# Kernel optimization log

Measured on AMD Instinct MI355X. Metric: run time of the kernel, lower is better.

Reference implementation:

```python
import jax, jax.numpy as jnp
import numpy as np

EPS = 1e-4  # F.normalize eps


def setup_inputs() -> dict:
    key = jax.random.key(0)
    k1, k2, k3, k4 = jax.random.split(key, 4)
    return {
        "pred_feat": jax.random.normal(k1, (8192, 6), dtype=jnp.float32),
        "pred_decoder": jax.random.normal(k2, (4096, 4), dtype=jnp.float32),
        "input_data": jax.random.normal(k3, (4096, 4), dtype=jnp.float32),
        "gt_data": jax.random.normal(k4, (32768, 6), dtype=jnp.float32),
    }


def _normalize(x, eps=EPS):
    # torch F.normalize: x / max(||x||, eps)
    n = jnp.linalg.norm(x, axis=1, keepdims=True)
    return x / jnp.maximum(n, eps)


def reference(pred_feat, pred_decoder, input_data, gt_data):
    # train_decoder=False path (default inference/encoder-training path)
    pred_points = pred_feat[:, :3]    # [N,3]
    pred_normals = pred_feat[:, 3:]   # [N,3]
    gt_points = gt_data[:, :3]        # [L,3]
    gt_normals = gt_data[:, 3:]       # [L,3]

    # Squared Euclidean distances; argmin over squared == argmin over cdist(p=2).
    # dists2: [N, L] -- the big memory-bound intermediate
    p2 = jnp.sum(pred_points * pred_points, axis=1, keepdims=True)   # [N,1]
    g2 = jnp.sum(gt_points * gt_points, axis=1)                       # [L]
    dists2 = p2 - 2.0 * (pred_points @ gt_points.T) + g2[None, :]
    min_indices = jnp.argmin(dists2, axis=1)                          # [N]

    matched_pts = gt_points[min_indices]                              # [N,3]
    inlier_loss = jnp.mean((pred_points - matched_pts) ** 2)

    matched_nrm = gt_normals[min_indices]                             # [N,3]
    cos_theta = jnp.sum(_normalize(pred_normals) * _normalize(matched_nrm), axis=1)
    norm_loss = jnp.mean(1.0 - cos_theta)

    return inlier_loss + norm_loss
```

## Files before the change

kernel.cpp:

```cpp
#include <hip/hip_runtime.h>
#include <float.h>

#define NPRED 8192
#define NGT   32768
#define BLK   256
#define P     8
#define NCHUNK (NPRED / (BLK * P))
#define NSEG   128
#define SEGLEN (NGT / NSEG)
#define G      4
#define NGRP   (SEGLEN / G)
#define NPB    (NPRED / BLK)


__global__ void prep_kernel(const float* __restrict__ gt, float4* __restrict__ gt4,
                            unsigned long long* __restrict__ res) {
    int j = blockIdx.x * blockDim.x + threadIdx.x;
    if (j < NGT) {
        float x = gt[j * 6 + 0], y = gt[j * 6 + 1], z = gt[j * 6 + 2];
        gt4[j] = make_float4(-2.0f * x, -2.0f * y, -2.0f * z, x * x + y * y + z * z);
    }
    if (j < NPRED) res[j] = 0xFFFFFFFFFFFFFFFFull;
}

__device__ __forceinline__ unsigned int fkey(float f) {
    unsigned int u = __float_as_uint(f);
    return u ^ (unsigned int)(((int)u >> 31) | 0x80000000);
}

__device__ __forceinline__ float score(const float4& g, float px, float py, float pz) {
    return fmaf(g.x, px, fmaf(g.y, py, fmaf(g.z, pz, g.w)));
}

__global__ __launch_bounds__(BLK, 2) void argmin_kernel(const float* __restrict__ pred,
                                                        const float4* __restrict__ gt4,
                                                        unsigned long long* __restrict__ res) {
    __shared__ float4 tile[SEGLEN];
    const int t = threadIdx.x;
    const int chunk = blockIdx.x;
    const int seg = blockIdx.y;
    const int j0 = seg * SEGLEN;

    tile[t] = gt4[j0 + t];

    float px[P], py[P], pz[P], best[P];
    int bg[P];
    const int pbase = chunk * (BLK * P) + t;
    #pragma unroll
    for (int k = 0; k < P; ++k) {
        const float* p = pred + (size_t)(pbase + k * BLK) * 6;
        px[k] = p[0]; py[k] = p[1]; pz[k] = p[2];
        best[k] = FLT_MAX; bg[k] = 0;
    }
    __syncthreads();

    #pragma unroll 2
    for (int grp = 0; grp < NGRP; ++grp) {
        float4 g0 = tile[grp * G + 0];
        float4 g1 = tile[grp * G + 1];
        float4 g2 = tile[grp * G + 2];
        float4 g3 = tile[grp * G + 3];
        #pragma unroll
        for (int k = 0; k < P; ++k) {
            float s0 = score(g0, px[k], py[k], pz[k]);
            float s1 = score(g1, px[k], py[k], pz[k]);
            float s2 = score(g2, px[k], py[k], pz[k]);
            float s3 = score(g3, px[k], py[k], pz[k]);
            float m = fminf(fminf(fminf(s0, s1), s2), s3);
            if (m < best[k]) { best[k] = m; bg[k] = grp; }
        }
    }

    #pragma unroll
    for (int k = 0; k < P; ++k) {
        int gb = bg[k] * G;
        float4 g0 = tile[gb + 0];
        float4 g1 = tile[gb + 1];
        float4 g2 = tile[gb + 2];
        float4 g3 = tile[gb + 3];
        float s0 = score(g0, px[k], py[k], pz[k]);
        float s1 = score(g1, px[k], py[k], pz[k]);
        float s2 = score(g2, px[k], py[k], pz[k]);
        int off = (s0 == best[k]) ? 0 : (s1 == best[k]) ? 1 : (s2 == best[k]) ? 2 : 3;
        (void)g3;
        unsigned long long pk = ((unsigned long long)fkey(best[k]) << 32)
                              | (unsigned long long)(j0 + gb + off);
        atomicMin(&res[pbase + k * BLK], pk);
    }
}

__global__ __launch_bounds__(BLK) void finalize_kernel(const float* __restrict__ pred,
                                                       const float* __restrict__ gt,
                                                       const unsigned long long* __restrict__ res,
                                                       float2* __restrict__ bsums) {
    int i = blockIdx.x * BLK + threadIdx.x;
    int bidx = (int)(res[i] & 0xFFFFFFFFull);

    const float* g = &gt[(size_t)bidx * 6];
    float gx = g[0], gy = g[1], gz = g[2];
    float gnx = g[3], gny = g[4], gnz = g[5];
    const float* p = &pred[(size_t)i * 6];
    float px = p[0], py = p[1], pz = p[2];
    float pnx = p[3], pny = p[4], pnz = p[5];

    float dx = px - gx, dy = py - gy, dz = pz - gz;
    float v1 = dx * dx + dy * dy + dz * dz;

    float pn = sqrtf(pnx * pnx + pny * pny + pnz * pnz);
    float gn = sqrtf(gnx * gnx + gny * gny + gnz * gnz);
    float denom = fmaxf(pn, 1e-4f) * fmaxf(gn, 1e-4f);
    float cosv = (pnx * gnx + pny * gny + pnz * gnz) / denom;
    float v2 = 1.0f - cosv;

    #pragma unroll
    for (int off = 32; off > 0; off >>= 1) {
        v1 += __shfl_down(v1, off);
        v2 += __shfl_down(v2, off);
    }
    __shared__ float s1[BLK / 64];
    __shared__ float s2[BLK / 64];
    int wid = threadIdx.x >> 6;
    if ((threadIdx.x & 63) == 0) { s1[wid] = v1; s2[wid] = v2; }
    __syncthreads();
    if (threadIdx.x == 0) {
        float a = 0.0f, b = 0.0f;
        #pragma unroll
        for (int w = 0; w < BLK / 64; ++w) { a += s1[w]; b += s2[w]; }
        bsums[blockIdx.x] = make_float2(a, b);
    }
}

__global__ void final_reduce_kernel(const float2* __restrict__ bsums, float* __restrict__ out) {
    int t = threadIdx.x;
    float v1 = 0.0f, v2 = 0.0f;
    if (t < NPB) { float2 r = bsums[t]; v1 = r.x; v2 = r.y; }
    #pragma unroll
    for (int off = 32; off > 0; off >>= 1) {
        v1 += __shfl_down(v1, off);
        v2 += __shfl_down(v2, off);
    }
    if (t == 0) out[0] = v1 / (NPRED * 3.0f) + v2 / (float)NPRED;
}

extern "C" void kernel_launch(void* const* d_in, const int* in_sizes, int n_in,
                              void* d_out, int out_size, void* d_ws, size_t ws_size,
                              hipStream_t stream) {
    const float* pred_feat = (const float*)d_in[0];
    const float* gt_data   = (const float*)d_in[3];
    float* out = (float*)d_out;

    char* ws = (char*)d_ws;
    float4* gt4 = (float4*)ws;
    unsigned long long* res = (unsigned long long*)(ws + (size_t)NGT * 16);
    float2* bsums = (float2*)(ws + (size_t)NGT * 16 + (size_t)NPRED * 8);

    prep_kernel<<<NGT / 256, 256, 0, stream>>>(gt_data, gt4, res);
    dim3 grid(NCHUNK, NSEG);
    argmin_kernel<<<grid, BLK, 0, stream>>>(pred_feat, gt4, res);
    finalize_kernel<<<NPB, BLK, 0, stream>>>(pred_feat, gt_data, res, bsums);
    final_reduce_kernel<<<1, 64, 0, stream>>>(bsums, out);
}
```

Before: 41.34 us.

## Retune argmin tiling and fuse final reduction via last-block counter

The argmin kernel now handles 4 predictions per thread instead of 8, with 8 GT points per group instead of 4, and the launch-bounds occupancy hint is raised to 4. This doubles the grid and is meant to lower register pressure so more waves stay resident. Separately, the final reduce kernel is removed: finalize blocks publish their partial sums with atomic stores, and the last block to arrive (tracked by an atomic counter reset in prep) computes the output. This saves one launch at the cost of atomics and a reset counter.

Result: faster. 39.26 us (-5.0%).

```diff
diff --git a/kernel.cpp b/kernel.cpp
--- a/kernel.cpp
+++ b/kernel.cpp
@@ -4,23 +4,26 @@
 #define NPRED 8192
 #define NGT   32768
 #define BLK   256
-#define P     8
+#define P     4
 #define NCHUNK (NPRED / (BLK * P))
 #define NSEG   128
 #define SEGLEN (NGT / NSEG)
-#define G      4
+#define G      8
 #define NGRP   (SEGLEN / G)
-#define NPB    (NPRED / BLK)
+#define FBLK   256
+#define NPB    (NPRED / FBLK)
 
 
 __global__ void prep_kernel(const float* __restrict__ gt, float4* __restrict__ gt4,
-                            unsigned long long* __restrict__ res) {
+                            unsigned long long* __restrict__ res,
+                            unsigned int* __restrict__ counter) {
     int j = blockIdx.x * blockDim.x + threadIdx.x;
     if (j < NGT) {
         float x = gt[j * 6 + 0], y = gt[j * 6 + 1], z = gt[j * 6 + 2];
         gt4[j] = make_float4(-2.0f * x, -2.0f * y, -2.0f * z, x * x + y * y + z * z);
     }
     if (j < NPRED) res[j] = 0xFFFFFFFFFFFFFFFFull;
+    if (j == 0) *counter = 0u;
 }
 
 __device__ __forceinline__ unsigned int fkey(float f) {
@@ -32,7 +35,7 @@
     return fmaf(g.x, px, fmaf(g.y, py, fmaf(g.z, pz, g.w)));
 }
 
-__global__ __launch_bounds__(BLK, 2) void argmin_kernel(const float* __restrict__ pred,
+__global__ __launch_bounds__(BLK, 4) void argmin_kernel(const float* __restrict__ pred,
                                                         const float4* __restrict__ gt4,
                                                         unsigned long long* __restrict__ res) {
     __shared__ float4 tile[SEGLEN];
@@ -54,46 +57,55 @@
     }
     __syncthreads();
 
-    #pragma unroll 2
+    #pragma unroll 1
     for (int grp = 0; grp < NGRP; ++grp) {
-        float4 g0 = tile[grp * G + 0];
-        float4 g1 = tile[grp * G + 1];
-        float4 g2 = tile[grp * G + 2];
-        float4 g3 = tile[grp * G + 3];
+        const int base = grp * G;
+        float4 g0 = tile[base + 0], g1 = tile[base + 1];
+        float4 g2 = tile[base + 2], g3 = tile[base + 3];
+        float4 g4 = tile[base + 4], g5 = tile[base + 5];
+        float4 g6 = tile[base + 6], g7 = tile[base + 7];
         #pragma unroll
         for (int k = 0; k < P; ++k) {
             float s0 = score(g0, px[k], py[k], pz[k]);
             float s1 = score(g1, px[k], py[k], pz[k]);
             float s2 = score(g2, px[k], py[k], pz[k]);
             float s3 = score(g3, px[k], py[k], pz[k]);
-            float m = fminf(fminf(fminf(s0, s1), s2), s3);
+            float s4 = score(g4, px[k], py[k], pz[k]);
+            float s5 = score(g5, px[k], py[k], pz[k]);
+            float s6 = score(g6, px[k], py[k], pz[k]);
+            float s7 = score(g7, px[k], py[k], pz[k]);
+            float t0 = fminf(fminf(s0, s1), s2);
+            float t1 = fminf(fminf(s3, s4), s5);
+            float t2 = fminf(fminf(s6, s7), t0);
+            float m  = fminf(t1, t2);
             if (m < best[k]) { best[k] = m; bg[k] = grp; }
         }
     }
 
     #pragma unroll
     for (int k = 0; k < P; ++k) {
-        int gb = bg[k] * G;
-        float4 g0 = tile[gb + 0];
-        float4 g1 = tile[gb + 1];
-        float4 g2 = tile[gb + 2];
-        float4 g3 = tile[gb + 3];
-        float s0 = score(g0, px[k], py[k], pz[k]);
-        float s1 = score(g1, px[k], py[k], pz[k]);
-        float s2 = score(g2, px[k], py[k], pz[k]);
-        int off = (s0 == best[k]) ? 0 : (s1 == best[k]) ? 1 : (s2 == best[k]) ? 2 : 3;
-        (void)g3;
+        const int gb = bg[k] * G;
+        float s[G];
+        #pragma unroll
+        for (int o = 0; o < G; ++o)
+            s[o] = score(tile[gb + o], px[k], py[k], pz[k]);
+        int off = G - 1;
+        #pragma unroll
+        for (int o = G - 2; o >= 0; --o)
+            if (s[o] == best[k]) off = o;
         unsigned long long pk = ((unsigned long long)fkey(best[k]) << 32)
                               | (unsigned long long)(j0 + gb + off);
         atomicMin(&res[pbase + k * BLK], pk);
     }
 }
 
-__global__ __launch_bounds__(BLK) void finalize_kernel(const float* __restrict__ pred,
-                                                       const float* __restrict__ gt,
-                                                       const unsigned long long* __restrict__ res,
-                                                       float2* __restrict__ bsums) {
-    int i = blockIdx.x * BLK + threadIdx.x;
+__global__ __launch_bounds__(FBLK) void finalize_kernel(const float* __restrict__ pred,
+                                                        const float* __restrict__ gt,
+                                                        const unsigned long long* __restrict__ res,
+                                                        unsigned long long* __restrict__ bsums,
+                                                        unsigned int* __restrict__ counter,
+                                                        float* __restrict__ out) {
+    int i = blockIdx.x * FBLK + threadIdx.x;
     int bidx = (int)(res[i] & 0xFFFFFFFFull);
 
     const float* g = &gt[(size_t)bidx * 6];
@@ -117,29 +129,38 @@
         v1 += __shfl_down(v1, off);
         v2 += __shfl_down(v2, off);
     }
-    __shared__ float s1[BLK / 64];
-    __shared__ float s2[BLK / 64];
+    __shared__ float s1[FBLK / 64];
+    __shared__ float s2[FBLK / 64];
+    __shared__ int lastFlag;
     int wid = threadIdx.x >> 6;
     if ((threadIdx.x & 63) == 0) { s1[wid] = v1; s2[wid] = v2; }
     __syncthreads();
     if (threadIdx.x == 0) {
         float a = 0.0f, b = 0.0f;
         #pragma unroll
-        for (int w = 0; w < BLK / 64; ++w) { a += s1[w]; b += s2[w]; }
-        bsums[blockIdx.x] = make_float2(a, b);
+        for (int w = 0; w < FBLK / 64; ++w) { a += s1[w]; b += s2[w]; }
+        unsigned long long pk = (unsigned long long)__float_as_uint(a)
+                              | ((unsigned long long)__float_as_uint(b) << 32);
+        __hip_atomic_store(&bsums[blockIdx.x], pk, __ATOMIC_RELEASE, __HIP_MEMORY_SCOPE_AGENT);
+        unsigned int tk = __hip_atomic_fetch_add(counter, 1u, __ATOMIC_ACQ_REL, __HIP_MEMORY_SCOPE_AGENT);
+        lastFlag = (tk == NPB - 1) ? 1 : 0;
     }
-}
-
-__global__ void final_reduce_kernel(const float2* __restrict__ bsums, float* __restrict__ out) {
-    int t = threadIdx.x;
-    float v1 = 0.0f, v2 = 0.0f;
-    if (t < NPB) { float2 r = bsums[t]; v1 = r.x; v2 = r.y; }
-    #pragma unroll
-    for (int off = 32; off > 0; off >>= 1) {
-        v1 += __shfl_down(v1, off);
-        v2 += __shfl_down(v2, off);
+    __syncthreads();
+    if (lastFlag && threadIdx.x < 64) {
+        float a = 0.0f, b = 0.0f;
+        if (threadIdx.x < NPB) {
+            unsigned long long pk = __hip_atomic_load(&bsums[threadIdx.x],
+                                                      __ATOMIC_ACQUIRE, __HIP_MEMORY_SCOPE_AGENT);
+            a = __uint_as_float((unsigned int)(pk & 0xFFFFFFFFull));
+            b = __uint_as_float((unsigned int)(pk >> 32));
+        }
+        #pragma unroll
+        for (int off = 32; off > 0; off >>= 1) {
+            a += __shfl_down(a, off);
+            b += __shfl_down(b, off);
+        }
+        if (threadIdx.x == 0) out[0] = a / (NPRED * 3.0f) + b / (float)NPRED;
     }
-    if (t == 0) out[0] = v1 / (NPRED * 3.0f) + v2 / (float)NPRED;
 }
 
 extern "C" void kernel_launch(void* const* d_in, const int* in_sizes, int n_in,
@@ -152,11 +173,11 @@
     char* ws = (char*)d_ws;
     float4* gt4 = (float4*)ws;
     unsigned long long* res = (unsigned long long*)(ws + (size_t)NGT * 16);
-    float2* bsums = (float2*)(ws + (size_t)NGT * 16 + (size_t)NPRED * 8);
+    unsigned long long* bsums = (unsigned long long*)(ws + (size_t)NGT * 16 + (size_t)NPRED * 8);
+    unsigned int* counter = (unsigned int*)(ws + (size_t)NGT * 16 + (size_t)NPRED * 8 + (size_t)NPB * 8);
 
-    prep_kernel<<<NGT / 256, 256, 0, stream>>>(gt_data, gt4, res);
+    prep_kernel<<<NGT / 256, 256, 0, stream>>>(gt_data, gt4, res, counter);
     dim3 grid(NCHUNK, NSEG);
     argmin_kernel<<<grid, BLK, 0, stream>>>(pred_feat, gt4, res);
-    finalize_kernel<<<NPB, BLK, 0, stream>>>(pred_feat, gt_data, res, bsums);
-    final_reduce_kernel<<<1, 64, 0, stream>>>(bsums, out);
+    finalize_kernel<<<NPB, FBLK, 0, stream>>>(pred_feat, gt_data, res, bsums, counter, out);
 }
```
